# Kernel optimization log

Measured on AMD Instinct MI355X. Metric: run time of the kernel, lower is better.

## Reference

```python
import jax, jax.numpy as jnp
import numpy as np

N_T, N_S, F_IN, H, N_OUT = 2048, 512, 7, 64, 3


def setup_inputs() -> dict:
    key = jax.random.key(0)
    ks = jax.random.split(key, 12)
    pts = jax.random.normal(ks[0], (N_T, 3), jnp.float32)
    centers = jax.random.normal(ks[1], (N_S, 3), jnp.float32)
    nrm = jax.random.normal(ks[2], (N_S, 3), jnp.float32)
    normals = nrm / jnp.linalg.norm(nrm, axis=-1, keepdims=True)
    areas = jax.random.uniform(ks[3], (N_S,), jnp.float32, 0.1, 1.0)
    ref_lengths = jax.random.uniform(ks[4], (2,), jnp.float32, 0.5, 1.5)

    def lin(k, i, o):
        return jax.random.normal(k, (i, o), jnp.float32) / np.float32(np.sqrt(i))

    return {
        "prediction_points": pts,
        "face_centers": centers,
        "face_normals": normals,
        "face_areas": areas,
        "reference_lengths": ref_lengths,
        "W1": lin(ks[5], F_IN, H), "b1": jnp.zeros((H,), jnp.float32),
        "W2": lin(ks[6], H, H),    "b2": jnp.zeros((H,), jnp.float32),
        "W3": lin(ks[7], H, H),    "b3": jnp.zeros((H,), jnp.float32),
        "Wout": lin(ks[8], H, N_OUT), "bout": jnp.zeros((N_OUT,), jnp.float32),
        "p_scale": jnp.float32(1.0), "p_bias": jnp.float32(0.0),
        "v_scale": jnp.float32(1.0), "v_bias": jnp.float32(0.0),
    }


def reference(prediction_points, face_centers, face_normals, face_areas,
              reference_lengths, W1, b1, W2, b2, W3, b3, Wout, bout,
              p_scale, p_bias, v_scale, v_bias):
    eps = jnp.float32(1e-8)
    # Pairwise relative geometry (translation/rotation-equivariant features).
    rvec = prediction_points[:, None, :] - face_centers[None, :, :]  # [T,S,3]
    r2 = jnp.sum(rvec * rvec, axis=-1)                               # [T,S]
    r = jnp.sqrt(r2 + eps)
    rhat = rvec / r[..., None]
    c = jnp.sum(rhat * face_normals[None, :, :], axis=-1)            # cos(angle)
    # Legendre polynomials P0..P3 (n_spherical_harmonics = 4).
    legendre = jnp.stack(
        [jnp.ones_like(c), c, 0.5 * (3.0 * c * c - 1.0),
         0.5 * (5.0 * c * c * c - 3.0 * c)], axis=-1)                # [T,S,4]
    # Multiscale nondimensional distance features, one per reference length.
    dfeat = 1.0 / (1.0 + r[..., None] / reference_lengths)           # [T,S,2]
    afeat = jnp.broadcast_to(jnp.log(face_areas)[None, :, None],
                             r.shape + (1,))                          # [T,S,1]
    feats = jnp.concatenate([dfeat, legendre, afeat], axis=-1)       # [T,S,7]
    # Kernel MLP evaluated per (target, source) pair.
    h = jnp.tanh(feats @ W1 + b1)
    h = jnp.tanh(h @ W2 + b2)
    h = jnp.tanh(h @ W3 + b3)
    out = h @ Wout + bout                                            # [T,S,3]
    # Green's-function-like decay, area-weighted boundary integral.
    decay = face_areas[None, :] / (r2 + 1.0)                         # [T,S]
    p = jnp.sum(out[..., 0] * decay, axis=1)                         # [T]
    vel = jnp.sum((out[..., 1:2] * rhat
                   + out[..., 2:3] * face_normals[None, :, :])
                  * decay[..., None], axis=1)                        # [T,3]
    pressure = p * p_scale + p_bias
    velocity = vel * v_scale + v_bias
    return jnp.concatenate([pressure[:, None], velocity], axis=-1)   # [T,4]
```

## Files before the change

kernel.cpp:

```cpp
#include <hip/hip_runtime.h>
#include <hip/hip_fp16.h>


#define N_T 2048
#define N_S 512
#define BLK 128
#define SCALE 2.885390081777927f

#define CPY_F 5888
#define CPY_U 1472

typedef _Float16 f16;
typedef _Float16 f16x4 __attribute__((ext_vector_type(4)));
typedef _Float16 f16x8 __attribute__((ext_vector_type(8)));
typedef float f32x4 __attribute__((ext_vector_type(4)));
typedef unsigned short u16;
typedef unsigned int u32;

__device__ __forceinline__ float zsig(float x) {
    float e = __builtin_amdgcn_exp2f(x);
    return __builtin_amdgcn_rcpf(e + 1.0f);
}

__device__ __forceinline__ f32x4 mfma16(f16x4 a, f16x4 b, f32x4 c) {
    return __builtin_amdgcn_mfma_f32_16x16x16f16(a, b, c, 0, 0, 0);
}
__device__ __forceinline__ f32x4 mfma32(f16x8 a, f16x8 b, f32x4 c) {
    return __builtin_amdgcn_mfma_f32_16x16x32_f16(a, b, c, 0, 0, 0);
}

__device__ __forceinline__ u32 pkrtz(float a, float b) {
    return __builtin_bit_cast(u32, __builtin_amdgcn_cvt_pkrtz(a, b));
}

__device__ __forceinline__ f16x4 lo4(uint4 g) {
    uint2 p; p.x = g.x; p.y = g.y;
    return __builtin_bit_cast(f16x4, p);
}
__device__ __forceinline__ f16x4 hi4(uint4 g) {
    uint2 p; p.x = g.z; p.y = g.w;
    return __builtin_bit_cast(f16x4, p);
}
__device__ __forceinline__ f16x8 all8(uint4 g) {
    return __builtin_bit_cast(f16x8, g);
}

__device__ __forceinline__ f16x8 tpack8(f32x4 cl, f32x4 ch) {
    uint4 p;
    p.x = pkrtz(zsig(cl[0]), zsig(cl[1]));
    p.y = pkrtz(zsig(cl[2]), zsig(cl[3]));
    p.z = pkrtz(zsig(ch[0]), zsig(ch[1]));
    p.w = pkrtz(zsig(ch[2]), zsig(ch[3]));
    return __builtin_bit_cast(f16x8, p);
}

__global__ __launch_bounds__(256) void prep_kernel(
    const float* __restrict__ W1, const float* __restrict__ b1,
    const float* __restrict__ W2, const float* __restrict__ b2,
    const float* __restrict__ W3, const float* __restrict__ b3,
    const float* __restrict__ Wout, const float* __restrict__ bout,
    float* __restrict__ ws)
{
    const int tid = blockIdx.x * 256 + threadIdx.x;
    if (tid < 5632) {
        const int cpy = tid / 1408;
        const int r   = tid - cpy * 1408;
        const int u   = r >> 6, lane = r & 63;
        const int q = lane >> 4, l15 = lane & 15;
        float x[8];
        bool lo = false;
        #pragma unroll
        for (int e = 0; e < 8; ++e) {
            const int half = e >> 2, j = e & 3;
            float v;
            if (u < 2) {
                const int mt = u * 2 + half;
                const int k = q * 4 + j;
                v = (k < 7) ? W1[k * 64 + mt * 16 + l15] * SCALE : 0.f;
            } else if (u < 10) {
                const int idx = u - 2, mt = idx >> 1, kp = idx & 1;
                const int k = (kp * 2 + half) * 16 + q * 4 + j;
                v = -2.0f * W2[k * 64 + mt * 16 + l15] * SCALE;
            } else if (u < 18) {
                const int idx = u - 10, mt = idx >> 1, kp = idx & 1;
                const int k = (kp * 2 + half) * 16 + q * 4 + j;
                v = -2.0f * W3[k * 64 + mt * 16 + l15] * SCALE;
            } else {
                const int kp = (u - 18) & 1;
                const int k = (kp * 2 + half) * 16 + q * 4 + j;
                v = (l15 < 3) ? -2.0f * Wout[k * 3 + l15] : 0.f;
                lo = (u >= 20);
            }
            x[e] = v;
        }
        u16 outw[8];
        #pragma unroll
        for (int e = 0; e < 8; ++e) {
            const f16 h = (f16)x[e];
            const f16 val = lo ? (f16)(x[e] - (float)h) : h;
            outw[e] = __builtin_bit_cast(u16, val);
        }
        uint4 g;
        g.x = outw[0] | ((u32)outw[1] << 16);
        g.y = outw[2] | ((u32)outw[3] << 16);
        g.z = outw[4] | ((u32)outw[5] << 16);
        g.w = outw[6] | ((u32)outw[7] << 16);
        *(uint4*)((char*)ws + (size_t)cpy * CPY_F * 4 + (size_t)(u * 64 + lane) * 16) = g;
    } else if (tid < 6412) {
        const int b = tid - 5632;
        const int cpy = b / 195, i = b - cpy * 195;
        if (i < 192) {
            const int Lb = i >> 6, j = i & 63;
            float bv;
            if (Lb == 0) {
                bv = b1[j];
            } else if (Lb == 1) {
                bv = b2[j];
                for (int k = 0; k < 64; ++k) bv += W2[k * 64 + j];
            } else {
                bv = b3[j];
                for (int k = 0; k < 64; ++k) bv += W3[k * 64 + j];
            }
            ws[cpy * CPY_F + 5632 + i] = bv * SCALE;
        } else {
            const int c3 = i - 192;
            float bv = bout[c3];
            for (int k = 0; k < 64; ++k) bv += Wout[k * 3 + c3];
            ws[cpy * CPY_F + 5824 + c3] = bv;
        }
    }
}

__global__ __launch_bounds__(BLK, 2) void globe_mfma(
    const float* __restrict__ pts, const float* __restrict__ ctr,
    const float* __restrict__ nrm, const float* __restrict__ areas,
    const float* __restrict__ rlen, const float* __restrict__ bout,
    const float* __restrict__ p_scale, const float* __restrict__ p_bias,
    const float* __restrict__ v_scale, const float* __restrict__ v_bias,
    const float* __restrict__ ws,
    float* __restrict__ out)
{
    __shared__ __align__(16) u16 featL[2][2][64][8];
    __shared__ __align__(16) uint4 geomL[2][2][64];
    __shared__ float xr[4];

    const int tid  = threadIdx.x;
    const int lane = tid & 63;
    const int wv   = tid >> 6;
    const int l15  = lane & 15;
    const int q    = lane >> 4;
    const int qf   = q & 1;
    const int t    = blockIdx.x;

    const float px = pts[3 * t + 0], py = pts[3 * t + 1], pz = pts[3 * t + 2];
    const float invL0 = __builtin_amdgcn_rcpf(rlen[0]);
    const float invL1 = __builtin_amdgcn_rcpf(rlen[1]);
    f32x4 co_init = (f32x4){0.f, 0.f, 0.f, 0.f};
    if (q == 0) { co_init[0] = ws[5824]; co_init[1] = ws[5825]; co_init[2] = ws[5826]; }

    const f16x4 bz = (f16x4){0, 0, 0, 0};
    float accp = 0.f, avx = 0.f, avy = 0.f, avz = 0.f;

    const int stag = (wv + (int)blockIdx.x) & 1;

    #pragma unroll 1
    for (int cc = 0; cc < 2; ++cc) {
        const int ch = cc ^ stag;
        const uint4* __restrict__ wsU = (const uint4*)ws + (ch * 2) * CPY_U;
        const float* __restrict__ wsBias = ws + (ch * 2) * CPY_F + 5632;

        #pragma unroll
        for (int st = 0; st < 2; ++st) {
            const int s = (wv * 4 + ch * 2 + st) * 64 + lane;
            const float cx = ctr[3 * s + 0], cy = ctr[3 * s + 1], cz = ctr[3 * s + 2];
            const float snx = nrm[3 * s + 0], sny = nrm[3 * s + 1], snz = nrm[3 * s + 2];
            const float ar = areas[s];
            const float rvx = px - cx, rvy = py - cy, rvz = pz - cz;
            const float r2 = rvx * rvx + rvy * rvy + rvz * rvz;
            const float r2e = r2 + 1e-8f;
            const float rinv = __builtin_amdgcn_rsqf(r2e);
            const float r = r2e * rinv;
            const float rhx = rvx * rinv, rhy = rvy * rinv, rhz = rvz * rinv;
            const float cth = rhx * snx + rhy * sny + rhz * snz;
            const float c2 = cth * cth;
            const float decay = ar * __builtin_amdgcn_rcpf(r2 + 1.0f);
            uint4 fw;
            fw.x = pkrtz(__builtin_amdgcn_rcpf(fmaf(r, invL0, 1.0f)),
                         __builtin_amdgcn_rcpf(fmaf(r, invL1, 1.0f)));
            fw.y = pkrtz(1.0f, cth);
            fw.z = pkrtz(fmaf(1.5f, c2, -0.5f), cth * fmaf(2.5f, c2, -1.5f));
            fw.w = pkrtz(__logf(ar), 0.0f);
            *(uint4*)&featL[wv][st][lane][0] = fw;
            uint4 g;
            g.x = __builtin_bit_cast(u32, decay);
            g.y = pkrtz(rhx, rhy);
            g.z = pkrtz(rhz, snx);
            g.w = pkrtz(sny, snz);
            geomL[wv][st][lane] = g;
        }

        f16x8 B2[2][2][4];
        {
            const uint4 g0 = wsU[0 * 64 + lane], g1 = wsU[1 * 64 + lane];
            f16x4 a1[4];
            a1[0] = lo4(g0); a1[1] = hi4(g0); a1[2] = lo4(g1); a1[3] = hi4(g1);
            float4 bv[4];
            #pragma unroll
            for (int mt = 0; mt < 4; ++mt)
                bv[mt] = *(const float4*)(wsBias + 0 * 64 + mt * 16 + q * 4);
            #pragma unroll
            for (int n4 = 0; n4 < 4; ++n4) {
                f16x4 bf[2];
                #pragma unroll
                for (int st = 0; st < 2; ++st) {
                    const f16x4 lv = *(const f16x4*)&featL[wv][st][n4 * 16 + l15][qf * 4];
                    bf[st] = (q < 2) ? lv : bz;
                }
                f32x4 c[2][4];
                #pragma unroll
                for (int mt = 0; mt < 4; ++mt) {
                    c[0][mt] = (f32x4){bv[mt].x, bv[mt].y, bv[mt].z, bv[mt].w};
                    c[1][mt] = c[0][mt];
                    c[0][mt] = mfma16(a1[mt], bf[0], c[0][mt]);
                    c[1][mt] = mfma16(a1[mt], bf[1], c[1][mt]);
                }
                #pragma unroll
                for (int kk = 0; kk < 2; ++kk) {
                    B2[0][kk][n4] = tpack8(c[0][2 * kk], c[0][2 * kk + 1]);
                    B2[1][kk][n4] = tpack8(c[1][2 * kk], c[1][2 * kk + 1]);
                }
            }
        }

        f16x8 B3[2][2][4];
        {
            f16x8 a[4][2];
            #pragma unroll
            for (int mt = 0; mt < 4; ++mt) {
                a[mt][0] = all8(wsU[(2 + 2 * mt) * 64 + lane]);
                a[mt][1] = all8(wsU[(3 + 2 * mt) * 64 + lane]);
            }
            float4 bv[4];
            #pragma unroll
            for (int mt = 0; mt < 4; ++mt)
                bv[mt] = *(const float4*)(wsBias + 1 * 64 + mt * 16 + q * 4);
            #pragma unroll
            for (int n4 = 0; n4 < 4; ++n4) {
                f32x4 c[2][4];
                #pragma unroll
                for (int mt = 0; mt < 4; ++mt) {
                    c[0][mt] = (f32x4){bv[mt].x, bv[mt].y, bv[mt].z, bv[mt].w};
                    c[1][mt] = c[0][mt];
                }
                #pragma unroll
                for (int kk = 0; kk < 2; ++kk)
                    #pragma unroll
                    for (int mt = 0; mt < 4; ++mt) {
                        c[0][mt] = mfma32(a[mt][kk], B2[0][kk][n4], c[0][mt]);
                        c[1][mt] = mfma32(a[mt][kk], B2[1][kk][n4], c[1][mt]);
                    }
                #pragma unroll
                for (int kk = 0; kk < 2; ++kk) {
                    B3[0][kk][n4] = tpack8(c[0][2 * kk], c[0][2 * kk + 1]);
                    B3[1][kk][n4] = tpack8(c[1][2 * kk], c[1][2 * kk + 1]);
                }
            }
        }

        f16x8 BO[2][2][4];
        {
            f16x8 a[4][2];
            #pragma unroll
            for (int mt = 0; mt < 4; ++mt) {
                a[mt][0] = all8(wsU[(10 + 2 * mt) * 64 + lane]);
                a[mt][1] = all8(wsU[(11 + 2 * mt) * 64 + lane]);
            }
            float4 bv[4];
            #pragma unroll
            for (int mt = 0; mt < 4; ++mt)
                bv[mt] = *(const float4*)(wsBias + 2 * 64 + mt * 16 + q * 4);
            #pragma unroll
            for (int n4 = 0; n4 < 4; ++n4) {
                f32x4 c[2][4];
                #pragma unroll
                for (int mt = 0; mt < 4; ++mt) {
                    c[0][mt] = (f32x4){bv[mt].x, bv[mt].y, bv[mt].z, bv[mt].w};
                    c[1][mt] = c[0][mt];
                }
                #pragma unroll
                for (int kk = 0; kk < 2; ++kk)
                    #pragma unroll
                    for (int mt = 0; mt < 4; ++mt) {
                        c[0][mt] = mfma32(a[mt][kk], B3[0][kk][n4], c[0][mt]);
                        c[1][mt] = mfma32(a[mt][kk], B3[1][kk][n4], c[1][mt]);
                    }
                #pragma unroll
                for (int kk = 0; kk < 2; ++kk) {
                    BO[0][kk][n4] = tpack8(c[0][2 * kk], c[0][2 * kk + 1]);
                    BO[1][kk][n4] = tpack8(c[1][2 * kk], c[1][2 * kk + 1]);
                }
            }
        }

        {
            const f16x8 aoh0 = all8(wsU[18 * 64 + lane]);
            const f16x8 aoh1 = all8(wsU[19 * 64 + lane]);
            const f16x8 aol0 = all8(wsU[20 * 64 + lane]);
            const f16x8 aol1 = all8(wsU[21 * 64 + lane]);
            #pragma unroll
            for (int n4 = 0; n4 < 4; ++n4) {
                f32x4 co[2];
                co[0] = co_init; co[1] = co_init;
                co[0] = mfma32(aoh0, BO[0][0][n4], co[0]);
                co[1] = mfma32(aoh0, BO[1][0][n4], co[1]);
                co[0] = mfma32(aol0, BO[0][0][n4], co[0]);
                co[1] = mfma32(aol0, BO[1][0][n4], co[1]);
                co[0] = mfma32(aoh1, BO[0][1][n4], co[0]);
                co[1] = mfma32(aoh1, BO[1][1][n4], co[1]);
                co[0] = mfma32(aol1, BO[0][1][n4], co[0]);
                co[1] = mfma32(aol1, BO[1][1][n4], co[1]);
                if (q == 0) {
                    #pragma unroll
                    for (int st = 0; st < 2; ++st) {
                        const uint4 g = geomL[wv][st][n4 * 16 + l15];
                        const float d = __builtin_bit_cast(float, g.x);
                        const float2 rxy = __half22float2(__builtin_bit_cast(__half2, g.y));
                        const float2 rzx = __half22float2(__builtin_bit_cast(__half2, g.z));
                        const float2 nyz = __half22float2(__builtin_bit_cast(__half2, g.w));
                        const float o0 = co[st][0], o1 = co[st][1], o2 = co[st][2];
                        accp = fmaf(o0, d, accp);
                        avx  = fmaf(fmaf(o1, rxy.x, o2 * rzx.y), d, avx);
                        avy  = fmaf(fmaf(o1, rxy.y, o2 * nyz.x), d, avy);
                        avz  = fmaf(fmaf(o1, rzx.x, o2 * nyz.y), d, avz);
                    }
                }
            }
        }
    }

    #pragma unroll
    for (int off = 8; off > 0; off >>= 1) {
        accp += __shfl_down(accp, off);
        avx  += __shfl_down(avx,  off);
        avy  += __shfl_down(avy,  off);
        avz  += __shfl_down(avz,  off);
    }

    if (wv == 1 && lane == 0) {
        xr[0] = accp; xr[1] = avx; xr[2] = avy; xr[3] = avz;
    }
    __syncthreads();
    if (wv == 0 && lane == 0) {
        accp += xr[0]; avx += xr[1]; avy += xr[2]; avz += xr[3];
        const float ps = p_scale[0], pb = p_bias[0];
        const float vs = v_scale[0], vb = v_bias[0];
        out[4 * t + 0] = fmaf(accp, ps, pb);
        out[4 * t + 1] = fmaf(avx, vs, vb);
        out[4 * t + 2] = fmaf(avy, vs, vb);
        out[4 * t + 3] = fmaf(avz, vs, vb);
    }
}

extern "C" void kernel_launch(void* const* d_in, const int* in_sizes, int n_in,
                              void* d_out, int out_size, void* d_ws, size_t ws_size,
                              hipStream_t stream) {
    (void)in_sizes; (void)n_in; (void)ws_size; (void)out_size;
    const float* pts   = (const float*)d_in[0];
    const float* ctr   = (const float*)d_in[1];
    const float* nrm   = (const float*)d_in[2];
    const float* areas = (const float*)d_in[3];
    const float* rlen  = (const float*)d_in[4];
    const float* W1    = (const float*)d_in[5];
    const float* b1    = (const float*)d_in[6];
    const float* W2    = (const float*)d_in[7];
    const float* b2    = (const float*)d_in[8];
    const float* W3    = (const float*)d_in[9];
    const float* b3    = (const float*)d_in[10];
    const float* Wout  = (const float*)d_in[11];
    const float* bout  = (const float*)d_in[12];
    const float* ps    = (const float*)d_in[13];
    const float* pb    = (const float*)d_in[14];
    const float* vs    = (const float*)d_in[15];
    const float* vb    = (const float*)d_in[16];
    float* ws = (float*)d_ws;

    prep_kernel<<<26, 256, 0, stream>>>(W1, b1, W2, b2, W3, b3, Wout, bout, ws);
    globe_mfma<<<N_T, BLK, 0, stream>>>(
        pts, ctr, nrm, areas, rlen, bout, ps, pb, vs, vb, ws, (float*)d_out);
}
```

Measured before the change: 132.2 us.

## Split each target across two single-wave blocks with atomic output accumulation

```diff
diff --git a/kernel.cpp b/kernel.cpp
--- a/kernel.cpp
+++ b/kernel.cpp
@@ -4,7 +4,7 @@
 
 #define N_T 2048
 #define N_S 512
-#define BLK 128
+#define BLK 64
 #define SCALE 2.885390081777927f
 
 #define CPY_F 5888
@@ -59,9 +59,10 @@
     const float* __restrict__ W2, const float* __restrict__ b2,
     const float* __restrict__ W3, const float* __restrict__ b3,
     const float* __restrict__ Wout, const float* __restrict__ bout,
-    float* __restrict__ ws)
+    float* __restrict__ ws, float* __restrict__ outp)
 {
     const int tid = blockIdx.x * 256 + threadIdx.x;
+    if (tid < 8192) outp[tid] = 0.f;
     if (tid < 5632) {
         const int cpy = tid / 1408;
         const int r   = tid - cpy * 1408;
@@ -140,17 +141,16 @@
     const float* __restrict__ ws,
     float* __restrict__ out)
 {
-    __shared__ __align__(16) u16 featL[2][2][64][8];
-    __shared__ __align__(16) uint4 geomL[2][2][64];
-    __shared__ float xr[4];
-
-    const int tid  = threadIdx.x;
-    const int lane = tid & 63;
-    const int wv   = tid >> 6;
+    __shared__ __align__(16) u16 featL[2][64][8];
+    __shared__ __align__(16) uint4 geomL[2][64];
+
+    const int lane = threadIdx.x & 63;
     const int l15  = lane & 15;
     const int q    = lane >> 4;
     const int qf   = q & 1;
-    const int t    = blockIdx.x;
+    const int b    = blockIdx.x;
+    const int t    = b >> 1;
+    const int h    = b & 1;
 
     const float px = pts[3 * t + 0], py = pts[3 * t + 1], pz = pts[3 * t + 2];
     const float invL0 = __builtin_amdgcn_rcpf(rlen[0]);
@@ -161,7 +161,7 @@
     const f16x4 bz = (f16x4){0, 0, 0, 0};
     float accp = 0.f, avx = 0.f, avy = 0.f, avz = 0.f;
 
-    const int stag = (wv + (int)blockIdx.x) & 1;
+    const int stag = (h + t) & 1;
 
     #pragma unroll 1
     for (int cc = 0; cc < 2; ++cc) {
@@ -171,7 +171,7 @@
 
         #pragma unroll
         for (int st = 0; st < 2; ++st) {
-            const int s = (wv * 4 + ch * 2 + st) * 64 + lane;
+            const int s = (h * 4 + ch * 2 + st) * 64 + lane;
             const float cx = ctr[3 * s + 0], cy = ctr[3 * s + 1], cz = ctr[3 * s + 2];
             const float snx = nrm[3 * s + 0], sny = nrm[3 * s + 1], snz = nrm[3 * s + 2];
             const float ar = areas[s];
@@ -190,13 +190,13 @@
             fw.y = pkrtz(1.0f, cth);
             fw.z = pkrtz(fmaf(1.5f, c2, -0.5f), cth * fmaf(2.5f, c2, -1.5f));
             fw.w = pkrtz(__logf(ar), 0.0f);
-            *(uint4*)&featL[wv][st][lane][0] = fw;
+            *(uint4*)&featL[st][lane][0] = fw;
             uint4 g;
             g.x = __builtin_bit_cast(u32, decay);
             g.y = pkrtz(rhx, rhy);
             g.z = pkrtz(rhz, snx);
             g.w = pkrtz(sny, snz);
-            geomL[wv][st][lane] = g;
+            geomL[st][lane] = g;
         }
 
         f16x8 B2[2][2][4];
@@ -213,7 +213,7 @@
                 f16x4 bf[2];
                 #pragma unroll
                 for (int st = 0; st < 2; ++st) {
-                    const f16x4 lv = *(const f16x4*)&featL[wv][st][n4 * 16 + l15][qf * 4];
+                    const f16x4 lv = *(const f16x4*)&featL[st][n4 * 16 + l15][qf * 4];
                     bf[st] = (q < 2) ? lv : bz;
                 }
                 f32x4 c[2][4];
@@ -322,7 +322,7 @@
                 if (q == 0) {
                     #pragma unroll
                     for (int st = 0; st < 2; ++st) {
-                        const uint4 g = geomL[wv][st][n4 * 16 + l15];
+                        const uint4 g = geomL[st][n4 * 16 + l15];
                         const float d = __builtin_bit_cast(float, g.x);
                         const float2 rxy = __half22float2(__builtin_bit_cast(__half2, g.y));
                         const float2 rzx = __half22float2(__builtin_bit_cast(__half2, g.z));
@@ -346,18 +346,14 @@
         avz  += __shfl_down(avz,  off);
     }
 
-    if (wv == 1 && lane == 0) {
-        xr[0] = accp; xr[1] = avx; xr[2] = avy; xr[3] = avz;
-    }
-    __syncthreads();
-    if (wv == 0 && lane == 0) {
-        accp += xr[0]; avx += xr[1]; avy += xr[2]; avz += xr[3];
-        const float ps = p_scale[0], pb = p_bias[0];
-        const float vs = v_scale[0], vb = v_bias[0];
-        out[4 * t + 0] = fmaf(accp, ps, pb);
-        out[4 * t + 1] = fmaf(avx, vs, vb);
-        out[4 * t + 2] = fmaf(avy, vs, vb);
-        out[4 * t + 3] = fmaf(avz, vs, vb);
+    if (lane == 0) {
+        const float ps = p_scale[0], vs = v_scale[0];
+        const float bp = h ? 0.f : p_bias[0];
+        const float bv = h ? 0.f : v_bias[0];
+        atomicAdd(&out[4 * t + 0], fmaf(accp, ps, bp));
+        atomicAdd(&out[4 * t + 1], fmaf(avx, vs, bv));
+        atomicAdd(&out[4 * t + 2], fmaf(avy, vs, bv));
+        atomicAdd(&out[4 * t + 3], fmaf(avz, vs, bv));
     }
 }
 
@@ -384,7 +380,8 @@
     const float* vb    = (const float*)d_in[16];
     float* ws = (float*)d_ws;
 
-    prep_kernel<<<26, 256, 0, stream>>>(W1, b1, W2, b2, W3, b3, Wout, bout, ws);
-    globe_mfma<<<N_T, BLK, 0, stream>>>(
+    prep_kernel<<<33, 256, 0, stream>>>(W1, b1, W2, b2, W3, b3, Wout, bout, ws,
+                                        (float*)d_out);
+    globe_mfma<<<N_T * 2, BLK, 0, stream>>>(
         pts, ctr, nrm, areas, rlen, bout, ps, pb, vs, vb, ws, (float*)d_out);
 }
```

Measured after the change: 130.6 us. About the same (-1.2%).
